# Optimization experiments

Measured on AMD Instinct MI355X. Metric: run time of the kernel, lower is better.

The kernel has to match this reference:

```python
import jax, jax.numpy as jnp
import numpy as np

B, N, F, S, OUT = 8, 12000, 128, 16, 128

def setup_inputs() -> dict:
    key = jax.random.key(0)
    k1, k2, k3, k4 = jax.random.split(key, 4)
    x = jax.random.normal(k1, (B, N, F), dtype=jnp.float32)
    # Linear(in_c*spiral_size, out_c): weight [out, in], bias [out]
    bound = 1.0 / np.sqrt(F * S)
    W = jax.random.uniform(k2, (OUT, F * S), dtype=jnp.float32, minval=-bound, maxval=bound)
    b = jax.random.uniform(k3, (OUT,), dtype=jnp.float32, minval=-bound, maxval=bound)
    spiral_adj = jax.random.randint(k4, (1, N, S), 0, N, dtype=jnp.int32)
    zero_padding = jnp.ones((1, N, 1), dtype=jnp.float32)
    return {"x": x, "W": W, "b": b, "spiral_adj": spiral_adj, "zero_padding": zero_padding}

def reference(x, W, b, spiral_adj, zero_padding):
    # x: [B, N, F]; spiral_adj: [1, N, S] vertex indices shared across batch
    idx = spiral_adj[0]                         # [N, S]
    spirals = x[:, idx, :]                      # [B, N, S, F] gather along vertex dim
    bsz, npts, s, f = spirals.shape
    spirals = spirals.reshape(bsz, npts, s * f)  # [B, N, S*F]
    out = jnp.einsum('bnk,ok->bno', spirals, W) + b  # [B, N, OUT]
    out = jax.nn.relu(out)
    return out * zero_padding
```

## Files before the change

### kernel.cpp

```cpp
#include <hip/hip_runtime.h>

#define BATCH 8
#define NPTS  12000
#define FDIM  128
#define SDIM  16
#define ODIM  128
#define KDIM  (SDIM * FDIM)
#define MTOT  (BATCH * NPTS)

#define BM 128
#define BK 64

#define NTILES 94
#define XELEMS (BATCH * NPTS * FDIM)
#define WELEMS (ODIM * KDIM)
#define XBYTES ((size_t)XELEMS * 2)
#define WBYTES ((size_t)WELEMS * 2)

typedef __bf16 bf16x4 __attribute__((ext_vector_type(4)));
typedef __bf16 bf16x8 __attribute__((ext_vector_type(8)));
typedef float  f32x4  __attribute__((ext_vector_type(4)));
typedef float  f32x8  __attribute__((ext_vector_type(8)));

#define AS1(p) ((const __attribute__((address_space(1))) void*)(p))
#define AS3(p) ((__attribute__((address_space(3))) void*)(p))

#define CVT_XBLK 6000
#define CVT_WBLK 128
#define CVT_BPB  750

__global__ __launch_bounds__(256)
void cvt_f32_bf16(const float* __restrict__ x, const float* __restrict__ W,
                  __bf16* __restrict__ xb, __bf16* __restrict__ Wb) {
    const int blk = blockIdx.x;
    const float* __restrict__ src;
    __bf16* __restrict__ dst;
    size_t base;
    if (blk < CVT_XBLK) {
        const int b = blk & 7;
        const int c = blk >> 3;
        base = ((size_t)b * CVT_BPB + c) * (256 * 8) + (size_t)threadIdx.x * 8;
        src = x;  dst = xb;
    } else {
        base = (size_t)(blk - CVT_XBLK) * (256 * 8) + (size_t)threadIdx.x * 8;
        src = W;  dst = Wb;
    }
    const f32x8 v = *reinterpret_cast<const f32x8*>(src + base);
    bf16x8 h;
#pragma unroll
    for (int e = 0; e < 8; ++e) h[e] = (__bf16)v[e];
    *reinterpret_cast<bf16x8*>(dst + base) = h;
}

__global__ __launch_bounds__(512, 4)
void spiral_gemm_bf16(const __bf16* __restrict__ xb,
                      const __bf16* __restrict__ Wb,
                      const float*  __restrict__ bias,
                      const int*    __restrict__ idx,
                      const float*  __restrict__ zp,
                      float*        __restrict__ out)
{
    __shared__ __bf16 As[2][BM * BK];
    __shared__ __bf16 Ws[2][ODIM * BK];
    __shared__ int    idxS[BM * SDIM];

    const int tid   = threadIdx.x;
    const int wave  = tid >> 6;
    const int lane  = tid & 63;
    const int batch = blockIdx.x & 7;
    const int n0    = (blockIdx.x >> 3) * BM;

    const int lrow8 = lane >> 3;
    const int clog  = (lane & 7) ^ lrow8;

    const __bf16* xbase = xb + (size_t)batch * (NPTS * FDIM);

    {
        const int row  = tid >> 2, q = tid & 3;
        const int n    = n0 + row;
        const int nrow = n < NPTS ? n : NPTS - 1;
        const int4* s4 = reinterpret_cast<const int4*>(idx + nrow * SDIM + q * 4);
        int4* d4       = reinterpret_cast<int4*>(&idxS[row * SDIM + q * 4]);
        d4[0] = s4[0];
    }
    __syncthreads();

    int rrow[2];
#pragma unroll
    for (int p = 0; p < 2; ++p) rrow[p] = (p * 8 + wave) * 8 + lrow8;

    int gCur[2], gNext[2];
#pragma unroll
    for (int p = 0; p < 2; ++p) gCur[p] = idxS[rrow[p] * SDIM + 0];

    auto issue = [&](int buf, int kt, const int* g) {
        const int f0 = (kt & 1) * BK;
#pragma unroll
        for (int p = 0; p < 2; ++p) {
            const int r0 = (p * 8 + wave) * 8;
            const __bf16* ga = xbase + (size_t)g[p] * FDIM + f0 + clog * 8;
            __builtin_amdgcn_global_load_lds(AS1(ga), AS3(&As[buf][r0 * BK]), 16, 0, 0);
            const __bf16* gw = Wb + (size_t)(r0 + lrow8) * KDIM + kt * BK + clog * 8;
            __builtin_amdgcn_global_load_lds(AS1(gw), AS3(&Ws[buf][r0 * BK]), 16, 0, 0);
        }
    };

    f32x4 acc[2][4];
#pragma unroll
    for (int i = 0; i < 2; ++i)
#pragma unroll
        for (int j = 0; j < 4; ++j)
            acc[i][j] = f32x4{0.f, 0.f, 0.f, 0.f};

    const int wm   = (wave >> 1) * 32;
    const int wn   = (wave & 1) * 64;
    const int lrow = lane & 15;
    const int quad = lane >> 4;

    auto compute = [&](int buf) {
#pragma unroll
        for (int kk = 0; kk < 2; ++kk) {
            const int ph = (kk * 4 + quad) ^ (lrow & 7);
            bf16x8 a[2], b[4];
#pragma unroll
            for (int i = 0; i < 2; ++i)
                a[i] = *reinterpret_cast<const bf16x8*>(
                    &As[buf][(wm + i * 16 + lrow) * BK + ph * 8]);
#pragma unroll
            for (int j = 0; j < 4; ++j)
                b[j] = *reinterpret_cast<const bf16x8*>(
                    &Ws[buf][(wn + j * 16 + lrow) * BK + ph * 8]);
#pragma unroll
            for (int i = 0; i < 2; ++i)
#pragma unroll
                for (int j = 0; j < 4; ++j)
                    acc[i][j] = __builtin_amdgcn_mfma_f32_16x16x32_bf16(
                        a[i], b[j], acc[i][j], 0, 0, 0);
        }
    };

    issue(0, 0, gCur);

    for (int t = 0; t < 16; ++t) {
        issue(1, 2 * t + 1, gCur);
        asm volatile("s_waitcnt vmcnt(4)" ::: "memory");
        asm volatile("s_barrier" ::: "memory");
        if (t < 15) {
#pragma unroll
            for (int p = 0; p < 2; ++p)
                gNext[p] = idxS[rrow[p] * SDIM + t + 1];
        }
        compute(0);
        asm volatile("s_barrier" ::: "memory");

        if (t < 15) {
            issue(0, 2 * t + 2, gNext);
            asm volatile("s_waitcnt vmcnt(4)" ::: "memory");
        } else {
            asm volatile("s_waitcnt vmcnt(0)" ::: "memory");
        }
        asm volatile("s_barrier" ::: "memory");
        compute(1);
        asm volatile("s_barrier" ::: "memory");
#pragma unroll
        for (int p = 0; p < 2; ++p) gCur[p] = gNext[p];
    }

#pragma unroll
    for (int i = 0; i < 2; ++i) {
#pragma unroll
        for (int r = 0; r < 4; ++r) {
            const int row = wm + i * 16 + quad * 4 + r;
            const int n   = n0 + row;
            if (n < NPTS) {
                const float z = zp[n];
                float* orow   = out + ((size_t)batch * NPTS + n) * ODIM;
#pragma unroll
                for (int j = 0; j < 4; ++j) {
                    const int col = wn + j * 16 + lrow;
                    float v = acc[i][j][r] + bias[col];
                    v = fmaxf(v, 0.f);
                    orow[col] = v * z;
                }
            }
        }
    }
}

#define LDA 72
__global__ __launch_bounds__(256, 2)
void spiral_gemm_fp32(const float* __restrict__ x, const float* __restrict__ W,
                      const float* __restrict__ bias, const int* __restrict__ idx,
                      const float* __restrict__ zp, float* __restrict__ out)
{
    __shared__ __bf16 Asf[BM * LDA];
    __shared__ __bf16 Wsf[ODIM * LDA];
    const int tid = threadIdx.x, wave = tid >> 6, lane = tid & 63;
    const int m0 = blockIdx.x * BM;
    const int srow = tid >> 3, schunk = tid & 7;
    int a_n[4]; const float* a_xb[4];
#pragma unroll
    for (int p = 0; p < 4; ++p) {
        int m = m0 + srow + p * 32, bb = m / NPTS;
        a_n[p] = m - bb * NPTS; a_xb[p] = x + (size_t)bb * (NPTS * FDIM);
    }
    f32x4 acc[4][4];
#pragma unroll
    for (int i = 0; i < 4; ++i)
#pragma unroll
        for (int j = 0; j < 4; ++j) acc[i][j] = f32x4{0.f,0.f,0.f,0.f};
    const int wm = (wave >> 1) * 64, wn = (wave & 1) * 64;
    const int lrow = lane & 15, quad = lane >> 4;
    for (int kt = 0; kt < KDIM / BK; ++kt) {
        const int s = kt >> 1, f0 = (kt & 1) * BK;
        __syncthreads();
#pragma unroll
        for (int p = 0; p < 4; ++p) {
            const int r = srow + p * 32;
            const int g = idx[a_n[p] * SDIM + s];
            const f32x8 v = *reinterpret_cast<const f32x8*>(
                a_xb[p] + (size_t)g * FDIM + f0 + schunk * 8);
            bf16x8 h;
#pragma unroll
            for (int e = 0; e < 8; ++e) h[e] = (__bf16)v[e];
            *reinterpret_cast<bf16x8*>(&Asf[r * LDA + schunk * 8]) = h;
            const f32x8 w = *reinterpret_cast<const f32x8*>(
                W + (size_t)r * KDIM + kt * BK + schunk * 8);
            bf16x8 hw;
#pragma unroll
            for (int e = 0; e < 8; ++e) hw[e] = (__bf16)w[e];
            *reinterpret_cast<bf16x8*>(&Wsf[r * LDA + schunk * 8]) = hw;
        }
        __syncthreads();
#pragma unroll
        for (int kk = 0; kk < 2; ++kk) {
            const int koff = kk * 32 + quad * 8;
            bf16x8 a[4], b[4];
#pragma unroll
            for (int i = 0; i < 4; ++i)
                a[i] = *reinterpret_cast<const bf16x8*>(&Asf[(wm + i*16 + lrow)*LDA + koff]);
#pragma unroll
            for (int j = 0; j < 4; ++j)
                b[j] = *reinterpret_cast<const bf16x8*>(&Wsf[(wn + j*16 + lrow)*LDA + koff]);
#pragma unroll
            for (int i = 0; i < 4; ++i)
#pragma unroll
                for (int j = 0; j < 4; ++j)
                    acc[i][j] = __builtin_amdgcn_mfma_f32_16x16x32_bf16(a[i], b[j], acc[i][j], 0,0,0);
        }
    }
#pragma unroll
    for (int i = 0; i < 4; ++i)
#pragma unroll
        for (int r = 0; r < 4; ++r) {
            const int row = wm + i * 16 + quad * 4 + r;
            const int m = m0 + row, bb = m / NPTS, nnn = m - bb * NPTS;
            const float z = zp[nnn];
            float* orow = out + (size_t)m * ODIM;
#pragma unroll
            for (int j = 0; j < 4; ++j) {
                const int col = wn + j * 16 + lrow;
                float v = acc[i][j][r] + bias[col];
                orow[col] = fmaxf(v, 0.f) * z;
            }
        }
}

extern "C" void kernel_launch(void* const* d_in, const int* in_sizes, int n_in,
                              void* d_out, int out_size, void* d_ws, size_t ws_size,
                              hipStream_t stream) {
    const float* x    = (const float*)d_in[0];
    const float* W    = (const float*)d_in[1];
    const float* bias = (const float*)d_in[2];
    const int*   idx  = (const int*)d_in[3];
    const float* zp   = (const float*)d_in[4];
    float*       out  = (float*)d_out;

    if (ws_size >= XBYTES + WBYTES) {
        __bf16* xb = (__bf16*)d_ws;
        __bf16* Wb = (__bf16*)((char*)d_ws + XBYTES);
        cvt_f32_bf16<<<dim3(CVT_XBLK + CVT_WBLK), dim3(256), 0, stream>>>(x, W, xb, Wb);
        spiral_gemm_bf16<<<dim3(BATCH * NTILES), dim3(512), 0, stream>>>(
            xb, Wb, bias, idx, zp, out);
    } else {
        spiral_gemm_fp32<<<dim3(MTOT / BM), dim3(256), 0, stream>>>(
            x, W, bias, idx, zp, out);
    }
}
```

Before: 156.6 us.

## Load gathered A fragments directly into registers instead of staging through LDS

The bf16 GEMM no longer stages the gathered x rows in shared memory. Each lane now loads its MFMA A-operand fragments straight from global memory into registers, double-buffered across the two K halves. W is still moved into LDS with asynchronous DMA. This cuts LDS traffic and footprint, which may allow more occupancy, but it makes each lane issue narrower, less coalesced gather loads and uses more registers. The fp32 fallback is only touched to rename constants.

```diff
diff --git a/kernel.cpp b/kernel.cpp
--- a/kernel.cpp
+++ b/kernel.cpp
@@ -60,7 +60,6 @@
                       const float*  __restrict__ zp,
                       float*        __restrict__ out)
 {
-    __shared__ __bf16 As[2][BM * BK];
     __shared__ __bf16 Ws[2][ODIM * BK];
     __shared__ int    idxS[BM * SDIM];
 
@@ -85,47 +84,50 @@
     }
     __syncthreads();
 
-    int rrow[2];
-#pragma unroll
-    for (int p = 0; p < 2; ++p) rrow[p] = (p * 8 + wave) * 8 + lrow8;
-
-    int gCur[2], gNext[2];
-#pragma unroll
-    for (int p = 0; p < 2; ++p) gCur[p] = idxS[rrow[p] * SDIM + 0];
-
-    auto issue = [&](int buf, int kt, const int* g) {
-        const int f0 = (kt & 1) * BK;
-#pragma unroll
-        for (int p = 0; p < 2; ++p) {
-            const int r0 = (p * 8 + wave) * 8;
-            const __bf16* ga = xbase + (size_t)g[p] * FDIM + f0 + clog * 8;
-            __builtin_amdgcn_global_load_lds(AS1(ga), AS3(&As[buf][r0 * BK]), 16, 0, 0);
-            const __bf16* gw = Wb + (size_t)(r0 + lrow8) * KDIM + kt * BK + clog * 8;
-            __builtin_amdgcn_global_load_lds(AS1(gw), AS3(&Ws[buf][r0 * BK]), 16, 0, 0);
-        }
-    };
-
-    f32x4 acc[2][4];
-#pragma unroll
-    for (int i = 0; i < 2; ++i)
-#pragma unroll
-        for (int j = 0; j < 4; ++j)
-            acc[i][j] = f32x4{0.f, 0.f, 0.f, 0.f};
-
     const int wm   = (wave >> 1) * 32;
     const int wn   = (wave & 1) * 64;
     const int lrow = lane & 15;
     const int quad = lane >> 4;
 
-    auto compute = [&](int buf) {
+    int arow[2];
+#pragma unroll
+    for (int i = 0; i < 2; ++i) arow[i] = wm + i * 16 + lrow;
+
+    int gCur[2], gNext[2];
+#pragma unroll
+    for (int i = 0; i < 2; ++i) gCur[i] = idxS[arow[i] * SDIM + 0];
+
+    auto aload = [&](bf16x8 (&a)[2][2], int f0, const int* g) {
+#pragma unroll
+        for (int i = 0; i < 2; ++i) {
+            const __bf16* ga = xbase + (size_t)g[i] * FDIM + f0 + quad * 8;
+#pragma unroll
+            for (int kk = 0; kk < 2; ++kk)
+                a[i][kk] = *reinterpret_cast<const bf16x8*>(ga + kk * 32);
+        }
+    };
+
+    auto dmaW = [&](int buf, int kt) {
+#pragma unroll
+        for (int p = 0; p < 2; ++p) {
+            const int r0 = (p * 8 + wave) * 8;
+            const __bf16* gw = Wb + (size_t)(r0 + lrow8) * KDIM + kt * BK + clog * 8;
+            __builtin_amdgcn_global_load_lds(AS1(gw), AS3(&Ws[buf][r0 * BK]), 16, 0, 0);
+        }
+    };
+
+    f32x4 acc[2][4];
+#pragma unroll
+    for (int i = 0; i < 2; ++i)
+#pragma unroll
+        for (int j = 0; j < 4; ++j)
+            acc[i][j] = f32x4{0.f, 0.f, 0.f, 0.f};
+
+    auto compute = [&](int buf, const bf16x8 (&a)[2][2]) {
 #pragma unroll
         for (int kk = 0; kk < 2; ++kk) {
             const int ph = (kk * 4 + quad) ^ (lrow & 7);
-            bf16x8 a[2], b[4];
-#pragma unroll
-            for (int i = 0; i < 2; ++i)
-                a[i] = *reinterpret_cast<const bf16x8*>(
-                    &As[buf][(wm + i * 16 + lrow) * BK + ph * 8]);
+            bf16x8 b[4];
 #pragma unroll
             for (int j = 0; j < 4; ++j)
                 b[j] = *reinterpret_cast<const bf16x8*>(
@@ -135,35 +137,42 @@
 #pragma unroll
                 for (int j = 0; j < 4; ++j)
                     acc[i][j] = __builtin_amdgcn_mfma_f32_16x16x32_bf16(
-                        a[i], b[j], acc[i][j], 0, 0, 0);
+                        a[i][kk], b[j], acc[i][j], 0, 0, 0);
         }
     };
 
-    issue(0, 0, gCur);
-
-    for (int t = 0; t < 16; ++t) {
-        issue(1, 2 * t + 1, gCur);
-        asm volatile("s_waitcnt vmcnt(4)" ::: "memory");
+    bf16x8 aA[2][2], aB[2][2];
+
+    aload(aA, 0, gCur);
+    dmaW(0, 0);
+
+    for (int u = 0; u < 16; ++u) {
+        aload(aB, BK, gCur);
+        dmaW(1, 2 * u + 1);
+        asm volatile("s_waitcnt vmcnt(6)" ::: "memory");
         asm volatile("s_barrier" ::: "memory");
-        if (t < 15) {
-#pragma unroll
-            for (int p = 0; p < 2; ++p)
-                gNext[p] = idxS[rrow[p] * SDIM + t + 1];
-        }
-        compute(0);
+        if (u < 15) {
+#pragma unroll
+            for (int i = 0; i < 2; ++i)
+                gNext[i] = idxS[arow[i] * SDIM + u + 1];
+        }
+        compute(0, aA);
         asm volatile("s_barrier" ::: "memory");
 
-        if (t < 15) {
-            issue(0, 2 * t + 2, gNext);
-            asm volatile("s_waitcnt vmcnt(4)" ::: "memory");
+        if (u < 15) {
+            aload(aA, 0, gNext);
+            dmaW(0, 2 * u + 2);
+            asm volatile("s_waitcnt vmcnt(6)" ::: "memory");
+            asm volatile("s_barrier" ::: "memory");
+            compute(1, aB);
+            asm volatile("s_barrier" ::: "memory");
+#pragma unroll
+            for (int i = 0; i < 2; ++i) gCur[i] = gNext[i];
         } else {
             asm volatile("s_waitcnt vmcnt(0)" ::: "memory");
-        }
-        asm volatile("s_barrier" ::: "memory");
-        compute(1);
-        asm volatile("s_barrier" ::: "memory");
-#pragma unroll
-        for (int p = 0; p < 2; ++p) gCur[p] = gNext[p];
+            asm volatile("s_barrier" ::: "memory");
+            compute(1, aB);
+        }
     }
 
 #pragma unroll
@@ -188,15 +197,16 @@
 }
 
 #define LDA 72
+#define BMF 128
 __global__ __launch_bounds__(256, 2)
 void spiral_gemm_fp32(const float* __restrict__ x, const float* __restrict__ W,
                       const float* __restrict__ bias, const int* __restrict__ idx,
                       const float* __restrict__ zp, float* __restrict__ out)
 {
-    __shared__ __bf16 Asf[BM * LDA];
+    __shared__ __bf16 Asf[BMF * LDA];
     __shared__ __bf16 Wsf[ODIM * LDA];
     const int tid = threadIdx.x, wave = tid >> 6, lane = tid & 63;
-    const int m0 = blockIdx.x * BM;
+    const int m0 = blockIdx.x * BMF;
     const int srow = tid >> 3, schunk = tid & 7;
     int a_n[4]; const float* a_xb[4];
 #pragma unroll
@@ -211,8 +221,8 @@
         for (int j = 0; j < 4; ++j) acc[i][j] = f32x4{0.f,0.f,0.f,0.f};
     const int wm = (wave >> 1) * 64, wn = (wave & 1) * 64;
     const int lrow = lane & 15, quad = lane >> 4;
-    for (int kt = 0; kt < KDIM / BK; ++kt) {
-        const int s = kt >> 1, f0 = (kt & 1) * BK;
+    for (int kt = 0; kt < KDIM / 64; ++kt) {
+        const int s = kt >> 1, f0 = (kt & 1) * 64;
         __syncthreads();
 #pragma unroll
         for (int p = 0; p < 4; ++p) {
@@ -225,7 +235,7 @@
             for (int e = 0; e < 8; ++e) h[e] = (__bf16)v[e];
             *reinterpret_cast<bf16x8*>(&Asf[r * LDA + schunk * 8]) = h;
             const f32x8 w = *reinterpret_cast<const f32x8*>(
-                W + (size_t)r * KDIM + kt * BK + schunk * 8);
+                W + (size_t)r * KDIM + kt * 64 + schunk * 8);
             bf16x8 hw;
 #pragma unroll
             for (int e = 0; e < 8; ++e) hw[e] = (__bf16)w[e];
@@ -283,7 +293,7 @@
         spiral_gemm_bf16<<<dim3(BATCH * NTILES), dim3(512), 0, stream>>>(
             xb, Wb, bias, idx, zp, out);
     } else {
-        spiral_gemm_fp32<<<dim3(MTOT / BM), dim3(256), 0, stream>>>(
+        spiral_gemm_fp32<<<dim3(MTOT / BMF), dim3(256), 0, stream>>>(
             x, W, bias, idx, zp, out);
     }
 }
```

Measured after the change: 209.5 us. 1.34x slower.

## Split K across wave pairs with 64x64 warp tiles and LDS reduction

Applied to the files above, without the earlier changes.

The bf16 GEMM kernel's 8 waves now form 4 pairs. Each pair owns a 64x64 output tile and its two waves each take half of every BK=64 slice. The larger per-wave tile raises MFMA work per LDS fragment load (4 A and 4 B fragments feeding 16 MFMAs). The two partial sums are combined through an LDS scratch buffer that reuses the A/W staging memory before the epilogue. The cost is more accumulator registers and an extra reduction phase with barriers, and only half the waves do the final store.

```diff
diff --git a/kernel.cpp b/kernel.cpp
--- a/kernel.cpp
+++ b/kernel.cpp
@@ -16,6 +16,8 @@
 #define WELEMS (ODIM * KDIM)
 #define XBYTES ((size_t)XELEMS * 2)
 #define WBYTES ((size_t)WELEMS * 2)
+
+#define SCW 68
 
 typedef __bf16 bf16x4 __attribute__((ext_vector_type(4)));
 typedef __bf16 bf16x8 __attribute__((ext_vector_type(8)));
@@ -60,9 +62,11 @@
                       const float*  __restrict__ zp,
                       float*        __restrict__ out)
 {
-    __shared__ __bf16 As[2][BM * BK];
-    __shared__ __bf16 Ws[2][ODIM * BK];
-    __shared__ int    idxS[BM * SDIM];
+    __shared__ char smem[73728];
+    auto As = reinterpret_cast<__bf16(*)[BM * BK]>(smem);
+    auto Ws = reinterpret_cast<__bf16(*)[ODIM * BK]>(smem + 32768);
+    int*   idxS    = reinterpret_cast<int*>(smem + 65536);
+    float* scratch = reinterpret_cast<float*>(smem);
 
     const int tid   = threadIdx.x;
     const int wave  = tid >> 6;
@@ -76,11 +80,11 @@
     const __bf16* xbase = xb + (size_t)batch * (NPTS * FDIM);
 
     {
-        const int row  = tid >> 2, q = tid & 3;
+        const int row  = tid >> 2, q4 = tid & 3;
         const int n    = n0 + row;
         const int nrow = n < NPTS ? n : NPTS - 1;
-        const int4* s4 = reinterpret_cast<const int4*>(idx + nrow * SDIM + q * 4);
-        int4* d4       = reinterpret_cast<int4*>(&idxS[row * SDIM + q * 4]);
+        const int4* s4 = reinterpret_cast<const int4*>(idx + nrow * SDIM + q4 * 4);
+        int4* d4       = reinterpret_cast<int4*>(&idxS[row * SDIM + q4 * 4]);
         d4[0] = s4[0];
     }
     __syncthreads();
@@ -105,38 +109,37 @@
         }
     };
 
-    f32x4 acc[2][4];
-#pragma unroll
-    for (int i = 0; i < 2; ++i)
+    f32x4 acc[4][4];
+#pragma unroll
+    for (int i = 0; i < 4; ++i)
 #pragma unroll
         for (int j = 0; j < 4; ++j)
             acc[i][j] = f32x4{0.f, 0.f, 0.f, 0.f};
 
-    const int wm   = (wave >> 1) * 32;
-    const int wn   = (wave & 1) * 64;
+    const int q    = wave >> 1;
+    const int kkw  = wave & 1;
+    const int wm   = (q >> 1) * 64;
+    const int wn   = (q & 1) * 64;
     const int lrow = lane & 15;
     const int quad = lane >> 4;
+    const int ph   = (kkw * 4 + quad) ^ (lrow & 7);
 
     auto compute = [&](int buf) {
-#pragma unroll
-        for (int kk = 0; kk < 2; ++kk) {
-            const int ph = (kk * 4 + quad) ^ (lrow & 7);
-            bf16x8 a[2], b[4];
-#pragma unroll
-            for (int i = 0; i < 2; ++i)
-                a[i] = *reinterpret_cast<const bf16x8*>(
-                    &As[buf][(wm + i * 16 + lrow) * BK + ph * 8]);
+        bf16x8 a[4], b[4];
+#pragma unroll
+        for (int i = 0; i < 4; ++i)
+            a[i] = *reinterpret_cast<const bf16x8*>(
+                &As[buf][(wm + i * 16 + lrow) * BK + ph * 8]);
+#pragma unroll
+        for (int j = 0; j < 4; ++j)
+            b[j] = *reinterpret_cast<const bf16x8*>(
+                &Ws[buf][(wn + j * 16 + lrow) * BK + ph * 8]);
+#pragma unroll
+        for (int i = 0; i < 4; ++i)
 #pragma unroll
             for (int j = 0; j < 4; ++j)
-                b[j] = *reinterpret_cast<const bf16x8*>(
-                    &Ws[buf][(wn + j * 16 + lrow) * BK + ph * 8]);
-#pragma unroll
-            for (int i = 0; i < 2; ++i)
-#pragma unroll
-                for (int j = 0; j < 4; ++j)
-                    acc[i][j] = __builtin_amdgcn_mfma_f32_16x16x32_bf16(
-                        a[i], b[j], acc[i][j], 0, 0, 0);
-        }
+                acc[i][j] = __builtin_amdgcn_mfma_f32_16x16x32_bf16(
+                    a[i], b[j], acc[i][j], 0, 0, 0);
     };
 
     issue(0, 0, gCur);
@@ -166,21 +169,41 @@
         for (int p = 0; p < 2; ++p) gCur[p] = gNext[p];
     }
 
-#pragma unroll
-    for (int i = 0; i < 2; ++i) {
-#pragma unroll
-        for (int r = 0; r < 4; ++r) {
-            const int row = wm + i * 16 + quad * 4 + r;
-            const int n   = n0 + row;
-            if (n < NPTS) {
-                const float z = zp[n];
-                float* orow   = out + ((size_t)batch * NPTS + n) * ODIM;
-#pragma unroll
-                for (int j = 0; j < 4; ++j) {
-                    const int col = wn + j * 16 + lrow;
-                    float v = acc[i][j][r] + bias[col];
-                    v = fmaxf(v, 0.f);
-                    orow[col] = v * z;
+    __syncthreads();
+    float* sc = scratch + q * (64 * SCW);
+    if (kkw == 1) {
+#pragma unroll
+        for (int i = 0; i < 4; ++i)
+#pragma unroll
+            for (int j = 0; j < 4; ++j)
+                *reinterpret_cast<f32x4*>(
+                    &sc[(j * 16 + lrow) * SCW + i * 16 + quad * 4]) = acc[i][j];
+    }
+    __syncthreads();
+    if (kkw == 0) {
+#pragma unroll
+        for (int i = 0; i < 4; ++i)
+#pragma unroll
+            for (int j = 0; j < 4; ++j)
+                acc[i][j] += *reinterpret_cast<const f32x4*>(
+                    &sc[(j * 16 + lrow) * SCW + i * 16 + quad * 4]);
+
+#pragma unroll
+        for (int i = 0; i < 4; ++i) {
+#pragma unroll
+            for (int r = 0; r < 4; ++r) {
+                const int row = wm + i * 16 + quad * 4 + r;
+                const int n   = n0 + row;
+                if (n < NPTS) {
+                    const float z = zp[n];
+                    float* orow   = out + ((size_t)batch * NPTS + n) * ODIM;
+#pragma unroll
+                    for (int j = 0; j < 4; ++j) {
+                        const int col = wn + j * 16 + lrow;
+                        float v = acc[i][j][r] + bias[col];
+                        v = fmaxf(v, 0.f);
+                        orow[col] = v * z;
+                    }
                 }
             }
         }
@@ -188,15 +211,16 @@
 }
 
 #define LDA 72
+#define BMF 128
 __global__ __launch_bounds__(256, 2)
 void spiral_gemm_fp32(const float* __restrict__ x, const float* __restrict__ W,
                       const float* __restrict__ bias, const int* __restrict__ idx,
                       const float* __restrict__ zp, float* __restrict__ out)
 {
-    __shared__ __bf16 Asf[BM * LDA];
+    __shared__ __bf16 Asf[BMF * LDA];
     __shared__ __bf16 Wsf[ODIM * LDA];
     const int tid = threadIdx.x, wave = tid >> 6, lane = tid & 63;
-    const int m0 = blockIdx.x * BM;
+    const int m0 = blockIdx.x * BMF;
     const int srow = tid >> 3, schunk = tid & 7;
     int a_n[4]; const float* a_xb[4];
 #pragma unroll
@@ -211,8 +235,8 @@
         for (int j = 0; j < 4; ++j) acc[i][j] = f32x4{0.f,0.f,0.f,0.f};
     const int wm = (wave >> 1) * 64, wn = (wave & 1) * 64;
     const int lrow = lane & 15, quad = lane >> 4;
-    for (int kt = 0; kt < KDIM / BK; ++kt) {
-        const int s = kt >> 1, f0 = (kt & 1) * BK;
+    for (int kt = 0; kt < KDIM / 64; ++kt) {
+        const int s = kt >> 1, f0 = (kt & 1) * 64;
         __syncthreads();
 #pragma unroll
         for (int p = 0; p < 4; ++p) {
@@ -225,7 +249,7 @@
             for (int e = 0; e < 8; ++e) h[e] = (__bf16)v[e];
             *reinterpret_cast<bf16x8*>(&Asf[r * LDA + schunk * 8]) = h;
             const f32x8 w = *reinterpret_cast<const f32x8*>(
-                W + (size_t)r * KDIM + kt * BK + schunk * 8);
+                W + (size_t)r * KDIM + kt * 64 + schunk * 8);
             bf16x8 hw;
 #pragma unroll
             for (int e = 0; e < 8; ++e) hw[e] = (__bf16)w[e];
@@ -283,7 +307,7 @@
         spiral_gemm_bf16<<<dim3(BATCH * NTILES), dim3(512), 0, stream>>>(
             xb, Wb, bias, idx, zp, out);
     } else {
-        spiral_gemm_fp32<<<dim3(MTOT / BM), dim3(256), 0, stream>>>(
+        spiral_gemm_fp32<<<dim3(MTOT / BMF), dim3(256), 0, stream>>>(
             x, W, bias, idx, zp, out);
     }
 }
```

Measured after the change: 157.8 us. About the same (+0.7%).
